# Optimization experiments

Measured on AMD Instinct MI355X. Metric: run time of the kernel, lower is better.

The kernel has to match this reference:

```python
import jax, jax.numpy as jnp
import numpy as np

SEQ, HID, IN, THETA = 4096, 512, 512, 5


def setup_inputs() -> dict:
    key = jax.random.key(0)
    k0, k1, k2, k3, k4 = jax.random.split(key, 5)
    return {
        "input": jax.random.normal(k0, (1, SEQ, IN), jnp.float32),
        "internal": jax.random.normal(k1, (THETA + 1, SEQ, HID), jnp.float32) * 0.1,
        "state": jnp.zeros((1, 1, HID), jnp.float32),
        "W_ih": jax.random.normal(k2, (HID, IN), jnp.float32) / np.sqrt(IN).astype(np.float32),
        "W_hh": jax.random.normal(k3, (HID, HID), jnp.float32) / np.sqrt(HID).astype(np.float32),
        "b": jax.random.normal(k4, (HID,), jnp.float32) * 0.01,
        "theta": THETA,
    }


def reference(input, internal, state, W_ih, W_hh, b, theta):
    # Unbatched path (batched=False), continuousTheta=False, trunc >= seq (no detach).
    # Cell: h' = tanh(x @ W_ih.T + h @ W_hh.T + b + noise); out = h'.
    x = input[0]                      # [S, I]
    pre_x = x @ W_ih.T + b            # [S, H] precompute input drive
    h0 = state[0, 0]                  # [H]

    # Main recurrence over the sequence (theta index 0 of internal drives it).
    def step(h, px_n):
        px, n = px_n
        h_new = jnp.tanh(px + h @ W_hh.T + n)
        return h_new, h_new

    _, hs = jax.lax.scan(step, h0, (pre_x, internal[0]))   # hs: [S, H]

    # Theta rollouts: padded input is zero, so drive = b + noise. The rollout at
    # every timestep starts from that timestep's main state -> vectorize over S
    # and scan over the theta axis.
    def roll(H, n):
        H_new = jnp.tanh(b + H @ W_hh.T + n)
        return H_new, H_new

    _, Hs = jax.lax.scan(roll, hs, internal[1:])           # Hs: [theta, S, H]

    outputs = jnp.concatenate([hs[None], Hs], axis=0)      # [theta+1, S, H]
    final_state = hs[-1][None, None]                        # [1, 1, H]
    return outputs, final_state
```

## Files before the change

### kernel.cpp

```cpp
#include <hip/hip_runtime.h>
#include <cstdint>
#include <cstddef>

#define SEQ 4096
#define HID 512
#define NTHETA 5
#define NBLK 8
#define SENT_BITS 0x40000000u

typedef unsigned long long u64;

__device__ __forceinline__ float tanh_fast(float x) {
  x = fminf(fmaxf(x, -20.0f), 20.0f);
  const float e = __expf(2.0f * x);
  return (e - 1.0f) / (e + 1.0f);
}

__device__ __forceinline__ float red16(float v) {
  int p;
  p = __builtin_amdgcn_update_dpp(0, __float_as_int(v), 0xB1, 0xF, 0xF, true);
  v += __int_as_float(p);
  p = __builtin_amdgcn_update_dpp(0, __float_as_int(v), 0x4E, 0xF, 0xF, true);
  v += __int_as_float(p);
  v += __int_as_float(__builtin_amdgcn_ds_swizzle(__float_as_int(v), 0x101F));
  v += __int_as_float(__builtin_amdgcn_ds_swizzle(__float_as_int(v), 0x201F));
  return v;
}

__device__ __forceinline__ int swz(int f) {
  return (f & ~7) | ((f ^ (f >> 3)) & 7);
}

__global__ __launch_bounds__(256) void gemm_bias_noise(
    const float* __restrict__ A, const float* __restrict__ W,
    const float* __restrict__ bias, const float* __restrict__ noise,
    float* __restrict__ C, int K, int doTanh)
{
  const int N = HID;
  const int bm = blockIdx.y, bn = blockIdx.x;
  const int tid = threadIdx.x;
  const int tx = tid & 15, ty = tid >> 4;
  const int row0 = bm * 64, col0 = bn * 64;
  __shared__ float As[16][68];
  __shared__ float Ws[16][68];
  float acc[4][4] = {{0.f, 0.f, 0.f, 0.f}, {0.f, 0.f, 0.f, 0.f},
                     {0.f, 0.f, 0.f, 0.f}, {0.f, 0.f, 0.f, 0.f}};
  const int lrow = tid >> 2, lkq = tid & 3;
  for (int kt = 0; kt < K; kt += 16) {
    const float4 av = *(const float4*)&A[(size_t)(row0 + lrow) * K + kt + lkq * 4];
    const float4 wv = *(const float4*)&W[(size_t)(col0 + lrow) * K + kt + lkq * 4];
    __syncthreads();
    As[lkq * 4 + 0][lrow] = av.x; As[lkq * 4 + 1][lrow] = av.y;
    As[lkq * 4 + 2][lrow] = av.z; As[lkq * 4 + 3][lrow] = av.w;
    Ws[lkq * 4 + 0][lrow] = wv.x; Ws[lkq * 4 + 1][lrow] = wv.y;
    Ws[lkq * 4 + 2][lrow] = wv.z; Ws[lkq * 4 + 3][lrow] = wv.w;
    __syncthreads();
#pragma unroll
    for (int k = 0; k < 16; ++k) {
      const float4 a = *(const float4*)&As[k][ty * 4];
      const float4 bq = *(const float4*)&Ws[k][tx * 4];
      const float a4[4] = {a.x, a.y, a.z, a.w};
      const float b4[4] = {bq.x, bq.y, bq.z, bq.w};
#pragma unroll
      for (int i = 0; i < 4; ++i)
#pragma unroll
        for (int j = 0; j < 4; ++j)
          acc[i][j] = fmaf(a4[i], b4[j], acc[i][j]);
    }
  }
  const float4 bv = *(const float4*)&bias[col0 + tx * 4];
#pragma unroll
  for (int i = 0; i < 4; ++i) {
    const int row = row0 + ty * 4 + i;
    const float4 nv = *(const float4*)&noise[(size_t)row * N + col0 + tx * 4];
    float4 o;
    o.x = acc[i][0] + bv.x + nv.x;
    o.y = acc[i][1] + bv.y + nv.y;
    o.z = acc[i][2] + bv.z + nv.z;
    o.w = acc[i][3] + bv.w + nv.w;
    if (doTanh) {
      o.x = tanh_fast(o.x); o.y = tanh_fast(o.y);
      o.z = tanh_fast(o.z); o.w = tanh_fast(o.w);
    }
    *(float4*)&C[(size_t)row * N + col0 + tx * 4] = o;
  }
}

__global__ void fill_sentinel(uint4* __restrict__ p, int n4) {
  const int i = blockIdx.x * blockDim.x + threadIdx.x;
  if (i < n4) p[i] = make_uint4(SENT_BITS, SENT_BITS, SENT_BITS, SENT_BITS);
}

__global__ __launch_bounds__(256) void recurrence(
    const float* __restrict__ Whh, const float* __restrict__ drive,
    const float* __restrict__ h0, unsigned* __restrict__ hexch)
{
  const int blk = blockIdx.x;
  const int base = blk * 64;
  const int tid = threadIdx.x;
  const int i = tid >> 4;
  const int j = tid & 15;

  __shared__ float hbuf[2][HID];

  float4 wv0[8], wv1[8], wv2[8], wv3[8];
#pragma unroll
  for (int c = 0; c < 8; ++c) {
    const size_t rb = (size_t)(base + 4 * i) * HID + 32 * j + 4 * c;
    wv0[c] = *(const float4*)&Whh[rb];
    wv1[c] = *(const float4*)&Whh[rb + HID];
    wv2[c] = *(const float4*)&Whh[rb + 2 * HID];
    wv3[c] = *(const float4*)&Whh[rb + 3 * HID];
  }

  const int fp = tid >> 1;
  const int woff = swz(fp) * 4 + (tid & 1) * 2;
  const bool own = (tid >= blk * 32) && (tid < blk * 32 + 32);

  const int zo = swz(16 * blk + i);

  for (int t = 0; t < SEQ; ++t) {
    const int buf = t & 1;

    float4 dv = make_float4(0.f, 0.f, 0.f, 0.f);
    if (j == 0)
      dv = *(const float4*)&drive[(size_t)t * HID + base + 4 * i];

    if (t == 0) {
      hbuf[0][woff]     = h0[2 * tid];
      hbuf[0][woff + 1] = h0[2 * tid + 1];
    } else if (!own) {
      const u64* src = (const u64*)&hexch[(size_t)(t - 1) * HID + 2 * tid];
      u64 u;
      do {
        u = __hip_atomic_load(src, __ATOMIC_RELAXED, __HIP_MEMORY_SCOPE_AGENT);
      } while ((unsigned)u == SENT_BITS || (unsigned)(u >> 32) == SENT_BITS);
      float2 hv;
      hv.x = __uint_as_float((unsigned)u);
      hv.y = __uint_as_float((unsigned)(u >> 32));
      *(float2*)&hbuf[buf][woff] = hv;
    }
    __syncthreads();
    asm volatile("" :: "v"(dv.x), "v"(dv.y), "v"(dv.z), "v"(dv.w));

    float a0 = 0.f, a1 = 0.f, a2 = 0.f, a3 = 0.f;
#pragma unroll
    for (int c = 0; c < 8; ++c) {
      const float4 h4 = *(const float4*)&hbuf[buf][(8 * j + ((c ^ j) & 7)) * 4];
      a0 = fmaf(wv0[c].x, h4.x, a0); a0 = fmaf(wv0[c].y, h4.y, a0);
      a0 = fmaf(wv0[c].z, h4.z, a0); a0 = fmaf(wv0[c].w, h4.w, a0);
      a1 = fmaf(wv1[c].x, h4.x, a1); a1 = fmaf(wv1[c].y, h4.y, a1);
      a1 = fmaf(wv1[c].z, h4.z, a1); a1 = fmaf(wv1[c].w, h4.w, a1);
      a2 = fmaf(wv2[c].x, h4.x, a2); a2 = fmaf(wv2[c].y, h4.y, a2);
      a2 = fmaf(wv2[c].z, h4.z, a2); a2 = fmaf(wv2[c].w, h4.w, a2);
      a3 = fmaf(wv3[c].x, h4.x, a3); a3 = fmaf(wv3[c].y, h4.y, a3);
      a3 = fmaf(wv3[c].z, h4.z, a3); a3 = fmaf(wv3[c].w, h4.w, a3);
    }
    a0 = red16(a0); a1 = red16(a1); a2 = red16(a2); a3 = red16(a3);

    if (j == 0) {
      const float y0 = tanh_fast(a0 + dv.x);
      const float y1 = tanh_fast(a1 + dv.y);
      const float y2 = tanh_fast(a2 + dv.z);
      const float y3 = tanh_fast(a3 + dv.w);
      unsigned* dst = &hexch[(size_t)t * HID + base + 4 * i];
      __hip_atomic_store(dst + 0, __float_as_uint(y0), __ATOMIC_RELAXED,
                         __HIP_MEMORY_SCOPE_AGENT);
      __hip_atomic_store(dst + 1, __float_as_uint(y1), __ATOMIC_RELAXED,
                         __HIP_MEMORY_SCOPE_AGENT);
      __hip_atomic_store(dst + 2, __float_as_uint(y2), __ATOMIC_RELAXED,
                         __HIP_MEMORY_SCOPE_AGENT);
      __hip_atomic_store(dst + 3, __float_as_uint(y3), __ATOMIC_RELAXED,
                         __HIP_MEMORY_SCOPE_AGENT);
      *(float4*)&hbuf[buf ^ 1][zo * 4] = make_float4(y0, y1, y2, y3);
    }
  }
}

__global__ void copy_final(const float* __restrict__ src, float* __restrict__ dst) {
  dst[threadIdx.x] = src[threadIdx.x];
}

extern "C" void kernel_launch(void* const* d_in, const int* in_sizes, int n_in,
                              void* d_out, int out_size, void* d_ws, size_t ws_size,
                              hipStream_t stream) {
  const float* input    = (const float*)d_in[0];
  const float* internal = (const float*)d_in[1];
  const float* state    = (const float*)d_in[2];
  const float* W_ih     = (const float*)d_in[3];
  const float* W_hh     = (const float*)d_in[4];
  const float* bias     = (const float*)d_in[5];
  float* out = (float*)d_out;

  const size_t plane = (size_t)SEQ * HID;
  unsigned* hexch = (unsigned*)out;
  float*    drive = out + 5 * plane;

  fill_sentinel<<<(SEQ * HID / 4 + 255) / 256, 256, 0, stream>>>(
      (uint4*)hexch, SEQ * HID / 4);

  dim3 gg(HID / 64, SEQ / 64);
  gemm_bias_noise<<<gg, 256, 0, stream>>>(input, W_ih, bias, internal, drive,
                                          HID, 0);
  recurrence<<<NBLK, 256, 0, stream>>>(W_hh, drive, state, hexch);
  for (int k = 0; k < NTHETA; ++k) {
    gemm_bias_noise<<<gg, 256, 0, stream>>>(out + (size_t)k * plane, W_hh, bias,
                                            internal + (size_t)(k + 1) * plane,
                                            out + (size_t)(k + 1) * plane,
                                            HID, 1);
  }
  copy_final<<<1, HID, 0, stream>>>(out + (size_t)4095 * HID, out + 6 * plane);
}
```

Before: 7.490 ms.

## Co-locate recurrence workers on one XCD and poll via L2-coherent loads

The recurrence grid now launches 256 blocks. Each block reads its XCC_ID and claims a slot per XCD with an atomic counter, and the first XCD to collect eight blocks becomes the worker set while every other block exits. Keeping all eight workers on one XCD lets the cross-block h exchange go through that XCD's shared L2. Polling therefore switches to sc0 loads, with a periodic agent-scope fallback, and stores are packed into 64-bit writes issued at both workgroup and agent scope. The cost is extra launch work, a memset for the claim counters, and reliance on undocumented coherence behaviour of sc0 loads within an XCD.

```diff
diff --git a/kernel.cpp b/kernel.cpp
--- a/kernel.cpp
+++ b/kernel.cpp
@@ -5,7 +5,7 @@
 #define SEQ 4096
 #define HID 512
 #define NTHETA 5
-#define NBLK 8
+#define NWRK 8
 #define SENT_BITS 0x40000000u
 
 typedef unsigned long long u64;
@@ -14,6 +14,13 @@
   x = fminf(fmaxf(x, -20.0f), 20.0f);
   const float e = __expf(2.0f * x);
   return (e - 1.0f) / (e + 1.0f);
+}
+
+__device__ __forceinline__ u64 load_sc0_u64(const u64* p) {
+  u64 u;
+  asm volatile("global_load_dwordx2 %0, %1, off sc0\n\ts_waitcnt vmcnt(0)"
+               : "=v"(u) : "v"(p) : "memory");
+  return u;
 }
 
 __device__ __forceinline__ float red16(float v) {
@@ -93,11 +100,36 @@
 
 __global__ __launch_bounds__(256) void recurrence(
     const float* __restrict__ Whh, const float* __restrict__ drive,
-    const float* __restrict__ h0, unsigned* __restrict__ hexch)
+    const float* __restrict__ h0, unsigned* __restrict__ hexch,
+    int* __restrict__ claim)
 {
-  const int blk = blockIdx.x;
-  const int base = blk * 64;
+  __shared__ int s_worker, s_slot;
   const int tid = threadIdx.x;
+
+  if (tid == 0) {
+    int xcd;
+    asm volatile("s_getreg_b32 %0, hwreg(HW_REG_XCC_ID)" : "=s"(xcd));
+    xcd &= 7;
+    const int slot = atomicAdd(&claim[xcd], 1);
+    if (slot == NWRK - 1) {
+      int expected = 0;
+      __hip_atomic_compare_exchange_strong(&claim[8], &expected, xcd + 1,
+                                           __ATOMIC_RELAXED, __ATOMIC_RELAXED,
+                                           __HIP_MEMORY_SCOPE_AGENT);
+    }
+    int ch;
+    do {
+      ch = __hip_atomic_load(&claim[8], __ATOMIC_RELAXED,
+                             __HIP_MEMORY_SCOPE_AGENT);
+    } while (ch == 0);
+    s_worker = (ch == xcd + 1 && slot < NWRK) ? 1 : 0;
+    s_slot = slot;
+  }
+  __syncthreads();
+  if (!s_worker) return;
+
+  const int slot = s_slot;
+  const int base = slot * 64;
   const int i = tid >> 4;
   const int j = tid & 15;
 
@@ -115,9 +147,9 @@
 
   const int fp = tid >> 1;
   const int woff = swz(fp) * 4 + (tid & 1) * 2;
-  const bool own = (tid >= blk * 32) && (tid < blk * 32 + 32);
-
-  const int zo = swz(16 * blk + i);
+  const bool own = (tid >= slot * 32) && (tid < slot * 32 + 32);
+
+  const int zo = swz(16 * slot + i);
 
   for (int t = 0; t < SEQ; ++t) {
     const int buf = t & 1;
@@ -131,10 +163,15 @@
       hbuf[0][woff + 1] = h0[2 * tid + 1];
     } else if (!own) {
       const u64* src = (const u64*)&hexch[(size_t)(t - 1) * HID + 2 * tid];
-      u64 u;
-      do {
-        u = __hip_atomic_load(src, __ATOMIC_RELAXED, __HIP_MEMORY_SCOPE_AGENT);
-      } while ((unsigned)u == SENT_BITS || (unsigned)(u >> 32) == SENT_BITS);
+      u64 u = load_sc0_u64(src);
+      int it = 0;
+      while ((unsigned)u == SENT_BITS || (unsigned)(u >> 32) == SENT_BITS) {
+        if ((++it & 63) == 0)
+          u = __hip_atomic_load(src, __ATOMIC_RELAXED,
+                                __HIP_MEMORY_SCOPE_AGENT);
+        else
+          u = load_sc0_u64(src);
+      }
       float2 hv;
       hv.x = __uint_as_float((unsigned)u);
       hv.y = __uint_as_float((unsigned)(u >> 32));
@@ -154,7 +191,7 @@
       a2 = fmaf(wv2[c].x, h4.x, a2); a2 = fmaf(wv2[c].y, h4.y, a2);
       a2 = fmaf(wv2[c].z, h4.z, a2); a2 = fmaf(wv2[c].w, h4.w, a2);
       a3 = fmaf(wv3[c].x, h4.x, a3); a3 = fmaf(wv3[c].y, h4.y, a3);
-      a3 = fmaf(wv3[c].z, h4.z, a3); a3 = fmaf(wv3[c].w, h4.w, a3);
+      a3 = fmaf(wv3[c].w, h4.w, a3); a3 = fmaf(wv3[c].z, h4.z, a3);
     }
     a0 = red16(a0); a1 = red16(a1); a2 = red16(a2); a3 = red16(a3);
 
@@ -163,14 +200,16 @@
       const float y1 = tanh_fast(a1 + dv.y);
       const float y2 = tanh_fast(a2 + dv.z);
       const float y3 = tanh_fast(a3 + dv.w);
-      unsigned* dst = &hexch[(size_t)t * HID + base + 4 * i];
-      __hip_atomic_store(dst + 0, __float_as_uint(y0), __ATOMIC_RELAXED,
+      u64* d64 = (u64*)&hexch[(size_t)t * HID + base + 4 * i];
+      const u64 p01 = (u64)__float_as_uint(y0) | ((u64)__float_as_uint(y1) << 32);
+      const u64 p23 = (u64)__float_as_uint(y2) | ((u64)__float_as_uint(y3) << 32);
+      __hip_atomic_store(d64 + 0, p01, __ATOMIC_RELAXED,
+                         __HIP_MEMORY_SCOPE_WORKGROUP);
+      __hip_atomic_store(d64 + 1, p23, __ATOMIC_RELAXED,
+                         __HIP_MEMORY_SCOPE_WORKGROUP);
+      __hip_atomic_store(d64 + 0, p01, __ATOMIC_RELAXED,
                          __HIP_MEMORY_SCOPE_AGENT);
-      __hip_atomic_store(dst + 1, __float_as_uint(y1), __ATOMIC_RELAXED,
-                         __HIP_MEMORY_SCOPE_AGENT);
-      __hip_atomic_store(dst + 2, __float_as_uint(y2), __ATOMIC_RELAXED,
-                         __HIP_MEMORY_SCOPE_AGENT);
-      __hip_atomic_store(dst + 3, __float_as_uint(y3), __ATOMIC_RELAXED,
+      __hip_atomic_store(d64 + 1, p23, __ATOMIC_RELAXED,
                          __HIP_MEMORY_SCOPE_AGENT);
       *(float4*)&hbuf[buf ^ 1][zo * 4] = make_float4(y0, y1, y2, y3);
     }
@@ -195,14 +234,16 @@
   const size_t plane = (size_t)SEQ * HID;
   unsigned* hexch = (unsigned*)out;
   float*    drive = out + 5 * plane;
-
+  int*      claim = (int*)d_ws;
+
+  hipMemsetAsync(d_ws, 0, 16 * sizeof(int), stream);
   fill_sentinel<<<(SEQ * HID / 4 + 255) / 256, 256, 0, stream>>>(
       (uint4*)hexch, SEQ * HID / 4);
 
   dim3 gg(HID / 64, SEQ / 64);
   gemm_bias_noise<<<gg, 256, 0, stream>>>(input, W_ih, bias, internal, drive,
                                           HID, 0);
-  recurrence<<<NBLK, 256, 0, stream>>>(W_hh, drive, state, hexch);
+  recurrence<<<256, 256, 0, stream>>>(W_hh, drive, state, hexch, claim);
   for (int k = 0; k < NTHETA; ++k) {
     gemm_bias_noise<<<gg, 256, 0, stream>>>(out + (size_t)k * plane, W_hh, bias,
                                             internal + (size_t)(k + 1) * plane,
```

New measurement: 28.05 ms. +274.5%, slower.
